# Kernel tuning notes

Hardware: AMD Instinct MI355X
Metric: run time of the kernel (lower is better)

Reference implementation:

```python
import jax, jax.numpy as jnp
import numpy as np

DIM = 512
HEADS = 8
DIM_HEAD = 64
HIDDEN = HEADS * DIM_HEAD  # 512


def setup_inputs() -> dict:
    key = jax.random.key(0)
    k1, k2, k3, k4 = jax.random.split(key, 4)
    x = jax.random.normal(k1, (8, DIM, 64, 64), dtype=jnp.float32)
    # 1x1 conv weights stored as [out_ch, in_ch] (kernel spatial dims are 1)
    w_qkv = jax.random.normal(k2, (HIDDEN * 3, DIM), dtype=jnp.float32) * (1.0 / np.sqrt(DIM))
    w_out = jax.random.normal(k3, (DIM, HIDDEN), dtype=jnp.float32) * (1.0 / np.sqrt(HIDDEN))
    b_out = jax.random.normal(k4, (DIM,), dtype=jnp.float32) * 0.01
    return {"x": x, "w_qkv": w_qkv, "w_out": w_out, "b_out": b_out}


def reference(x, w_qkv, w_out, b_out):
    b, c, h, w = x.shape
    n = h * w
    # to_qkv: 1x1 conv == per-pixel GEMM over channels
    qkv = jnp.einsum('bchw,oc->bohw', x, w_qkv)            # [b, 3*hidden, h, w]
    qkv = qkv.reshape(b, 3, HEADS, DIM_HEAD, n)            # matches torch reshape order
    q, k, v = qkv[:, 0], qkv[:, 1], qkv[:, 2]              # each [b, heads, dim_head, n]
    k = jax.nn.softmax(k, axis=-1)                          # softmax over spatial positions
    context = jnp.einsum('bhdn,bhen->bhde', k, v)          # [b, heads, d, e] kv outer-product
    out = jnp.einsum('bhde,bhdn->bhen', context, q)        # query readout [b, heads, e, n]
    out = out.reshape(b, HEADS * DIM_HEAD, h, w)
    # to_out: 1x1 conv with bias
    return jnp.einsum('bchw,oc->bohw', out, w_out) + b_out[None, :, None, None]
```

## Files before the change

### kernel.cpp

```cpp
#include <hip/hip_runtime.h>
#include <hip/hip_bf16.h>
#include <math.h>

#define NB    8
#define CDIM  512
#define NSP   4096
#define NHEAD 8

typedef short short8 __attribute__((ext_vector_type(8)));
typedef float f32x4  __attribute__((ext_vector_type(4)));

__device__ __forceinline__ unsigned short f2bf(float f) {
    unsigned int u = __float_as_uint(f);
    u += 0x7fff + ((u >> 16) & 1);
    return (unsigned short)(u >> 16);
}
__device__ __forceinline__ float bf2f(unsigned short s) {
    return __uint_as_float(((unsigned int)s) << 16);
}
__device__ __forceinline__ void gld_lds16(const void* g, void* s) {
    __builtin_amdgcn_global_load_lds(
        (const __attribute__((address_space(1))) unsigned int*)g,
        (__attribute__((address_space(3))) unsigned int*)s, 16, 0, 0);
}
__device__ __forceinline__ void split8(const float* s, short8& hi, short8& lo) {
    float4 a = *reinterpret_cast<const float4*>(s);
    float4 b = *reinterpret_cast<const float4*>(s + 4);
    float v[8] = {a.x, a.y, a.z, a.w, b.x, b.y, b.z, b.w};
    #pragma unroll
    for (int j = 0; j < 8; ++j) {
        unsigned short hh = f2bf(v[j]);
        hi[j] = (short)hh;
        lo[j] = (short)f2bf(v[j] - bf2f(hh));
    }
}

__global__ __launch_bounds__(256) void convert_x(const float* __restrict__ x,
    unsigned short* __restrict__ xh, unsigned short* __restrict__ xl)
{
    const int cb4 = blockIdx.x;
    const int kt  = blockIdx.y;
    const int b   = blockIdx.z;
    const int tid = threadIdx.x;

    __shared__ float sx[32][65];

    const int r  = tid >> 3;
    const int c8 = (tid & 7) * 8;
    const float* xp = x + ((long)b * CDIM + kt * 32 + r) * NSP + cb4 * 64 + c8;
    float4 v0 = *reinterpret_cast<const float4*>(xp);
    float4 v1 = *reinterpret_cast<const float4*>(xp + 4);
    sx[r][c8 + 0] = v0.x; sx[r][c8 + 1] = v0.y; sx[r][c8 + 2] = v0.z; sx[r][c8 + 3] = v0.w;
    sx[r][c8 + 4] = v1.x; sx[r][c8 + 5] = v1.y; sx[r][c8 + 6] = v1.z; sx[r][c8 + 7] = v1.w;
    __syncthreads();

    const int cb_l  = tid >> 6;
    const int lane  = tid & 63;
    const int cb    = cb4 * 4 + cb_l;
    const int col_l = cb_l * 16 + (lane & 15);
    const int k0    = (lane >> 4) * 8;
    short8 hv, lv;
    #pragma unroll
    for (int j = 0; j < 8; ++j) {
        float v = sx[k0 + j][col_l];
        unsigned short hh = f2bf(v);
        hv[j] = (short)hh;
        lv[j] = (short)f2bf(v - bf2f(hh));
    }
    const long base = (((long)(b * 256 + cb) * 16 + kt) * 512) + lane * 8;
    *reinterpret_cast<short8*>(xh + base) = hv;
    *reinterpret_cast<short8*>(xl + base) = lv;
}

__global__ __launch_bounds__(64) void convert_w(const float* __restrict__ w,
    unsigned short* __restrict__ wh, unsigned short* __restrict__ wl)
{
    const int lane = threadIdx.x & 63;
    const int rb = blockIdx.x;
    const int kt = blockIdx.y;
    const int row = rb * 16 + (lane & 15);
    const int k0  = kt * 32 + (lane >> 4) * 8;
    const float* wp = w + (long)row * CDIM + k0;
    const long base = ((long)rb * 16 + kt) * 512 + lane * 8;
    short8 hv, lv;
    #pragma unroll
    for (int j = 0; j < 8; ++j) {
        float v = wp[j];
        unsigned short h = f2bf(v);
        hv[j] = (short)h;
        lv[j] = (short)f2bf(v - bf2f(h));
    }
    *reinterpret_cast<short8*>(wh + base) = hv;
    *reinterpret_cast<short8*>(wl + base) = lv;
}

__global__ __launch_bounds__(64) void convert_b(const float* __restrict__ src,
    int ld, unsigned short* __restrict__ bh, unsigned short* __restrict__ bl)
{
    const int lane = threadIdx.x & 63;
    const int cb = blockIdx.x;
    const int kt = blockIdx.y;
    const int col = cb * 16 + (lane & 15);
    const int k0  = kt * 32 + (lane >> 4) * 8;
    const float* sp = src + (long)k0 * ld + col;
    const long base = ((long)cb * 16 + kt) * 512 + lane * 8;
    short8 hv, lv;
    #pragma unroll
    for (int j = 0; j < 8; ++j) {
        float v = sp[(long)j * ld];
        unsigned short h = f2bf(v);
        hv[j] = (short)h;
        lv[j] = (short)f2bf(v - bf2f(h));
    }
    *reinterpret_cast<short8*>(bh + base) = hv;
    *reinterpret_cast<short8*>(bl + base) = lv;
}

__global__ __launch_bounds__(256, 2) void fused_kv_ctx(
    const unsigned short* __restrict__ Ah, const unsigned short* __restrict__ Al,
    const unsigned short* __restrict__ Bh, const unsigned short* __restrict__ Bl,
    float* __restrict__ ctx, float* __restrict__ ssum)
{
    const int ch = blockIdx.x;
    const int h  = blockIdx.y;
    const int b  = blockIdx.z;
    const int tid  = threadIdx.x;
    const int lane = tid & 63;
    const int wid  = tid >> 6;
    const int wr = wid >> 1, wc = wid & 1;

    __shared__ __align__(16) char lds[49152];

    f32x4 acc[4][8];
    #pragma unroll
    for (int m = 0; m < 4; ++m)
        #pragma unroll
        for (int n = 0; n < 8; ++n)
            acc[m][n] = (f32x4){0.f, 0.f, 0.f, 0.f};

    const unsigned short* srcs[12];
    #pragma unroll
    for (int i = 0; i < 12; ++i) {
        const int blk = wid * 12 + i;
        const unsigned short* s;
        if (blk < 16) {
            const int sub = blk & 7;
            const int rb = (sub < 4) ? (h * 4 + sub) : (32 + h * 4 + (sub - 4));
            s = ((blk < 8) ? Ah : Al) + ((long)(rb * 16) << 9);
        } else {
            const int j = (blk - 16) & 15;
            const int cb = ch * 16 + j;
            s = ((blk < 32) ? Bh : Bl) + (((long)(b * 256 + cb) * 16) << 9);
        }
        srcs[i] = s + lane * 8;
    }

    for (int kt = 0; kt < 16; ++kt) {
        #pragma unroll
        for (int i = 0; i < 12; ++i) {
            gld_lds16(srcs[i], lds + (wid * 12 + i) * 1024);
            srcs[i] += 512;
        }
        __syncthreads();

        short8 ah[4], al[4];
        #pragma unroll
        for (int m = 0; m < 4; ++m) {
            ah[m] = *reinterpret_cast<const short8*>(lds +        (wr * 4 + m) * 1024 + lane * 16);
            al[m] = *reinterpret_cast<const short8*>(lds + 8192 + (wr * 4 + m) * 1024 + lane * 16);
        }
        #pragma unroll
        for (int n = 0; n < 8; ++n) {
            short8 bh = *reinterpret_cast<const short8*>(lds + 16384 + (wc * 8 + n) * 1024 + lane * 16);
            short8 bl = *reinterpret_cast<const short8*>(lds + 32768 + (wc * 8 + n) * 1024 + lane * 16);
            #pragma unroll
            for (int m = 0; m < 4; ++m) {
                acc[m][n] = __builtin_amdgcn_mfma_f32_16x16x32_bf16(ah[m], bh, acc[m][n], 0, 0, 0);
                acc[m][n] = __builtin_amdgcn_mfma_f32_16x16x32_bf16(ah[m], bl, acc[m][n], 0, 0, 0);
                acc[m][n] = __builtin_amdgcn_mfma_f32_16x16x32_bf16(al[m], bh, acc[m][n], 0, 0, 0);
            }
        }
        __syncthreads();
    }

    if (wr == 0) {
        #pragma unroll
        for (int m = 0; m < 4; ++m)
            #pragma unroll
            for (int j = 0; j < 4; ++j) {
                float s = 0.f;
                #pragma unroll
                for (int n = 0; n < 8; ++n) {
                    float e = __expf(acc[m][n][j]);
                    acc[m][n][j] = e;
                    s += e;
                }
                s += __shfl_xor(s, 1); s += __shfl_xor(s, 2);
                s += __shfl_xor(s, 4); s += __shfl_xor(s, 8);
                if ((lane & 15) == 0)
                    atomicAdd(&ssum[b * 512 + h * 64 + m * 16 + (lane >> 4) * 4 + j], s);
            }
    }

    float* Plds = (float*)lds;
    float* Vlds = (float*)(lds + 64 * 68 * 4);
    f32x4 acc2[2][2];
    #pragma unroll
    for (int mi = 0; mi < 2; ++mi)
        #pragma unroll
        for (int ni = 0; ni < 2; ++ni) acc2[mi][ni] = (f32x4){0.f, 0.f, 0.f, 0.f};

    #pragma unroll
    for (int q = 0; q < 4; ++q) {
        __syncthreads();
        if (wc == (q >> 1)) {
            float* T = (wr == 0) ? Plds : Vlds;
            #pragma unroll
            for (int m = 0; m < 4; ++m)
                #pragma unroll
                for (int nn = 0; nn < 4; ++nn)
                    #pragma unroll
                    for (int j = 0; j < 4; ++j)
                        T[(m * 16 + (lane >> 4) * 4 + j) * 68 + nn * 16 + (lane & 15)]
                            = acc[m][(q & 1) * 4 + nn][j];
        }
        __syncthreads();

        #pragma unroll
        for (int ks = 0; ks < 2; ++ks) {
            const int kcol = ks * 32 + (lane >> 4) * 8;
            short8 pa_h[2], pa_l[2], vb_h[2], vb_l[2];
            #pragma unroll
            for (int mi = 0; mi < 2; ++mi)
                split8(&Plds[((wr * 2 + mi) * 16 + (lane & 15)) * 68 + kcol], pa_h[mi], pa_l[mi]);
            #pragma unroll
            for (int ni = 0; ni < 2; ++ni)
                split8(&Vlds[((wc * 2 + ni) * 16 + (lane & 15)) * 68 + kcol], vb_h[ni], vb_l[ni]);
            #pragma unroll
            for (int mi = 0; mi < 2; ++mi)
                #pragma unroll
                for (int ni = 0; ni < 2; ++ni) {
                    acc2[mi][ni] = __builtin_amdgcn_mfma_f32_16x16x32_bf16(pa_h[mi], vb_h[ni], acc2[mi][ni], 0, 0, 0);
                    acc2[mi][ni] = __builtin_amdgcn_mfma_f32_16x16x32_bf16(pa_h[mi], vb_l[ni], acc2[mi][ni], 0, 0, 0);
                    acc2[mi][ni] = __builtin_amdgcn_mfma_f32_16x16x32_bf16(pa_l[mi], vb_h[ni], acc2[mi][ni], 0, 0, 0);
                }
        }
    }

    float* cp = ctx + (long)(b * NHEAD + h) * 4096;
    #pragma unroll
    for (int mi = 0; mi < 2; ++mi)
        #pragma unroll
        for (int ni = 0; ni < 2; ++ni) {
            const int d0 = (wr * 2 + mi) * 16;
            const int e0 = (wc * 2 + ni) * 16;
            #pragma unroll
            for (int j = 0; j < 4; ++j)
                atomicAdd(&cp[(d0 + (lane >> 4) * 4 + j) * 64 + e0 + (lane & 15)], acc2[mi][ni][j]);
        }
}

template<int NKT, bool BIAS>
__global__ __launch_bounds__(512, 2) void gemm_mfma256(
    const unsigned short* __restrict__ Ah, const unsigned short* __restrict__ Al,
    const unsigned short* __restrict__ Bh, const unsigned short* __restrict__ Bl,
    float* __restrict__ C, const float* __restrict__ bias,
    int N, int aBatchRB, int bBatchCB, long cBatch)
{
    const int b    = blockIdx.z;
    const int tid  = threadIdx.x;
    const int lane = tid & 63;
    const int wid  = tid >> 6;
    const int wr   = wid >> 2;
    const int wc   = wid & 3;

    __shared__ __align__(16) char lds[2][65536];

    f32x4 acc[8][4];
    #pragma unroll
    for (int m = 0; m < 8; ++m)
        #pragma unroll
        for (int n = 0; n < 4; ++n)
            acc[m][n] = (f32x4){0.f, 0.f, 0.f, 0.f};

    const int rb0 = b * aBatchRB + blockIdx.y * 16;
    const int cb0 = b * bBatchCB + blockIdx.x * 16;

    const unsigned short* srcs[8];
    #pragma unroll
    for (int i = 0; i < 8; ++i) {
        const int blk = wid * 8 + i;
        const int sub = blk & 15;
        const unsigned short* s;
        if (blk < 16)      s = Ah + ((long)(rb0 + sub) * NKT << 9);
        else if (blk < 32) s = Al + ((long)(rb0 + sub) * NKT << 9);
        else if (blk < 48) s = Bh + ((long)(cb0 + sub) * NKT << 9);
        else               s = Bl + ((long)(cb0 + sub) * NKT << 9);
        srcs[i] = s + lane * 8;
    }
    const int ldsoff = wid * 8192;

    #pragma unroll
    for (int i = 0; i < 8; ++i) {
        gld_lds16(srcs[i], &lds[0][ldsoff + i * 1024]);
        srcs[i] += 512;
    }

    int cur = 0;
    for (int kt = 0; kt < NKT; ++kt) {
        if (kt + 1 < NKT) {
            #pragma unroll
            for (int i = 0; i < 8; ++i) {
                gld_lds16(srcs[i], &lds[cur ^ 1][ldsoff + i * 1024]);
                srcs[i] += 512;
            }
            asm volatile("s_waitcnt vmcnt(8)" ::: "memory");
        } else {
            asm volatile("s_waitcnt vmcnt(0)" ::: "memory");
        }
        __builtin_amdgcn_s_barrier();

        const char* L = lds[cur];
        short8 ah[8], al[8];
        #pragma unroll
        for (int m = 0; m < 8; ++m) {
            ah[m] = *reinterpret_cast<const short8*>(L +         (wr * 8 + m) * 1024 + lane * 16);
            al[m] = *reinterpret_cast<const short8*>(L + 16384 + (wr * 8 + m) * 1024 + lane * 16);
        }
        __builtin_amdgcn_s_setprio(1);
        #pragma unroll
        for (int n = 0; n < 4; ++n) {
            short8 bh = *reinterpret_cast<const short8*>(L + 32768 + (wc * 4 + n) * 1024 + lane * 16);
            short8 bl = *reinterpret_cast<const short8*>(L + 49152 + (wc * 4 + n) * 1024 + lane * 16);
            #pragma unroll
            for (int m = 0; m < 8; ++m) {
                acc[m][n] = __builtin_amdgcn_mfma_f32_16x16x32_bf16(ah[m], bh, acc[m][n], 0, 0, 0);
                acc[m][n] = __builtin_amdgcn_mfma_f32_16x16x32_bf16(ah[m], bl, acc[m][n], 0, 0, 0);
                acc[m][n] = __builtin_amdgcn_mfma_f32_16x16x32_bf16(al[m], bh, acc[m][n], 0, 0, 0);
            }
        }
        __builtin_amdgcn_s_setprio(0);
        asm volatile("" ::: "memory");
        __builtin_amdgcn_s_barrier();
        asm volatile("" ::: "memory");
        cur ^= 1;
    }

    const int row0 = blockIdx.y * 256 + wr * 128;
    const int col0 = blockIdx.x * 256 + wc * 64;
    float* Cb = C + (long)b * cBatch;
    #pragma unroll
    for (int m = 0; m < 8; ++m)
        #pragma unroll
        for (int n = 0; n < 4; ++n) {
            const int col = col0 + n * 16 + (lane & 15);
            #pragma unroll
            for (int j = 0; j < 4; ++j) {
                const int row = row0 + m * 16 + (lane >> 4) * 4 + j;
                float v = acc[m][n][j];
                if (BIAS) v += bias[row];
                Cb[(long)row * N + col] = v;
            }
        }
}

template<int NKT, bool BIAS>
__global__ __launch_bounds__(256) void gemm_mfma(
    const unsigned short* __restrict__ Ah, const unsigned short* __restrict__ Al,
    const unsigned short* __restrict__ Bh, const unsigned short* __restrict__ Bl,
    float* __restrict__ C, const float* __restrict__ bias,
    int N, int aBatchRB, int bBatchCB, long cBatch)
{
    const int b    = blockIdx.z;
    const int tid  = threadIdx.x;
    const int lane = tid & 63;
    const int wid  = tid >> 6;
    const int wr   = wid >> 1;
    const int wc   = wid & 1;

    __shared__ __align__(16) char lds[32768];

    f32x4 acc[4][4];
    #pragma unroll
    for (int m = 0; m < 4; ++m)
        #pragma unroll
        for (int n = 0; n < 4; ++n)
            acc[m][n] = (f32x4){0.f, 0.f, 0.f, 0.f};

    const int rb0 = b * aBatchRB + blockIdx.y * 8;
    const int cb0 = b * bBatchCB + blockIdx.x * 8;

    const unsigned short* srcs[8];
    #pragma unroll
    for (int i = 0; i < 8; ++i) {
        const int blk = wid * 8 + i;
        const int sub = blk & 7;
        const unsigned short* s;
        if (blk < 8)       s = Ah + ((long)(rb0 + sub) * NKT << 9);
        else if (blk < 16) s = Al + ((long)(rb0 + sub) * NKT << 9);
        else if (blk < 24) s = Bh + ((long)(cb0 + sub) * NKT << 9);
        else               s = Bl + ((long)(cb0 + sub) * NKT << 9);
        srcs[i] = s + lane * 8;
    }

    for (int kt = 0; kt < NKT; ++kt) {
        #pragma unroll
        for (int i = 0; i < 8; ++i) {
            gld_lds16(srcs[i], lds + (wid * 8 + i) * 1024);
            srcs[i] += 512;
        }
        __syncthreads();

        short8 ah[4], al[4], bh[4], bl[4];
        #pragma unroll
        for (int m = 0; m < 4; ++m) {
            ah[m] = *reinterpret_cast<const short8*>(lds +         (wr * 4 + m) * 1024 + lane * 16);
            al[m] = *reinterpret_cast<const short8*>(lds +  8192 + (wr * 4 + m) * 1024 + lane * 16);
        }
        #pragma unroll
        for (int n = 0; n < 4; ++n) {
            bh[n] = *reinterpret_cast<const short8*>(lds + 16384 + (wc * 4 + n) * 1024 + lane * 16);
            bl[n] = *reinterpret_cast<const short8*>(lds + 24576 + (wc * 4 + n) * 1024 + lane * 16);
        }
        #pragma unroll
        for (int m = 0; m < 4; ++m)
            #pragma unroll
            for (int n = 0; n < 4; ++n) {
                acc[m][n] = __builtin_amdgcn_mfma_f32_16x16x32_bf16(ah[m], bh[n], acc[m][n], 0, 0, 0);
                acc[m][n] = __builtin_amdgcn_mfma_f32_16x16x32_bf16(ah[m], bl[n], acc[m][n], 0, 0, 0);
                acc[m][n] = __builtin_amdgcn_mfma_f32_16x16x32_bf16(al[m], bh[n], acc[m][n], 0, 0, 0);
            }
        __syncthreads();
    }

    const int row0 = blockIdx.y * 128 + wr * 64;
    const int col0 = blockIdx.x * 128 + wc * 64;
    float* Cb = C + (long)b * cBatch;
    #pragma unroll
    for (int m = 0; m < 4; ++m)
        #pragma unroll
        for (int n = 0; n < 4; ++n) {
            const int col = col0 + n * 16 + (lane & 15);
            #pragma unroll
            for (int j = 0; j < 4; ++j) {
                const int row = row0 + m * 16 + (lane >> 4) * 4 + j;
                float v = acc[m][n][j];
                if (BIAS) v += bias[row];
                Cb[(long)row * N + col] = v;
            }
        }
}

__global__ __launch_bounds__(256) void zero_buf(float* p, int n) {
    for (int i = blockIdx.x * 256 + threadIdx.x; i < n; i += gridDim.x * 256) p[i] = 0.f;
}

__global__ __launch_bounds__(256) void ctx_fold(
    const float* __restrict__ w_out, const float* __restrict__ ctx,
    const float* __restrict__ ssum, float* __restrict__ Amat)
{
    const int o0 = blockIdx.x * 64;
    const int h  = blockIdx.y;
    const int b  = blockIdx.z;
    const int tid = threadIdx.x;

    __shared__ float Wo[64][65];
    __shared__ float Ct[64][65];

    for (int idx = tid; idx < 64 * 16; idx += 256) {
        const int r = idx >> 4;
        const int c = (idx & 15) * 4;
        float4 w4 = *reinterpret_cast<const float4*>(&w_out[(long)(o0 + r) * CDIM + h * 64 + c]);
        Wo[r][c + 0] = w4.x; Wo[r][c + 1] = w4.y; Wo[r][c + 2] = w4.z; Wo[r][c + 3] = w4.w;
        float4 c4 = *reinterpret_cast<const float4*>(&ctx[(((long)(b * NHEAD + h) * 64 + r) * 64) + c]);
        Ct[r][c + 0] = c4.x; Ct[r][c + 1] = c4.y; Ct[r][c + 2] = c4.z; Ct[r][c + 3] = c4.w;
    }
    __syncthreads();

    const int to = tid >> 4, td = tid & 15;
    float acc[4][4];
    #pragma unroll
    for (int i = 0; i < 4; ++i)
        #pragma unroll
        for (int j = 0; j < 4; ++j) acc[i][j] = 0.f;

    for (int e = 0; e < 64; ++e) {
        float ro[4], rd[4];
        #pragma unroll
        for (int i = 0; i < 4; ++i) ro[i] = Wo[to * 4 + i][e];
        #pragma unroll
        for (int j = 0; j < 4; ++j) rd[j] = Ct[td * 4 + j][e];
        #pragma unroll
        for (int i = 0; i < 4; ++i)
            #pragma unroll
            for (int j = 0; j < 4; ++j) acc[i][j] += ro[i] * rd[j];
    }

    #pragma unroll
    for (int i = 0; i < 4; ++i)
        #pragma unroll
        for (int j = 0; j < 4; ++j) {
            const float s = 1.f / ssum[b * 512 + h * 64 + td * 4 + j];
            Amat[(long)b * CDIM * CDIM + (long)(o0 + to * 4 + i) * CDIM + h * 64 + td * 4 + j]
                = acc[i][j] * s;
        }
}

extern "C" void kernel_launch(void* const* d_in, const int* in_sizes, int n_in,
                              void* d_out, int out_size, void* d_ws, size_t ws_size,
                              hipStream_t stream) {
    (void)in_sizes; (void)n_in; (void)out_size; (void)ws_size;
    const float* x     = (const float*)d_in[0];
    const float* w_qkv = (const float*)d_in[1];
    const float* w_out = (const float*)d_in[2];
    const float* b_out = (const float*)d_in[3];
    float* out = (float*)d_out;

    char* ws = (char*)d_ws;
    unsigned short* xh   = (unsigned short*)(ws + 134217728L);
    unsigned short* xl   = (unsigned short*)(ws + 167772160L);
    unsigned short* wkvh = (unsigned short*)(ws + 201326592L);
    unsigned short* wkvl = (unsigned short*)(ws + 202375168L);
    float*          ssum = (float*)(ws + 203423744L);
    float*          ctx  = (float*)(ws + 203440128L);
    float*          Amat = (float*)(ws);
    float*          W3   = (float*)(ws + 8388608L);
    unsigned short* amh  = (unsigned short*)(ws + 16777216L);
    unsigned short* aml  = (unsigned short*)(ws + 20971520L);
    unsigned short* wqh  = (unsigned short*)(ws + 25165824L);
    unsigned short* wql  = (unsigned short*)(ws + 26214400L);
    unsigned short* w3h  = (unsigned short*)(ws + 27262976L);
    unsigned short* w3l  = (unsigned short*)(ws + 31457280L);

    convert_x<<<dim3(64, 16, NB), 256, 0, stream>>>(x, xh, xl);
    convert_w<<<dim3(64, 16), 64, 0, stream>>>(w_qkv + 512L * CDIM, wkvh, wkvl);
    zero_buf<<<256, 256, 0, stream>>>(ssum, (16384 + 1048576) / 4);

    fused_kv_ctx<<<dim3(16, NHEAD, NB), 256, 0, stream>>>(
        wkvh, wkvl, xh, xl, ctx, ssum);

    convert_b<<<dim3(32, 16), 64, 0, stream>>>(w_qkv, CDIM, wqh, wql);

    ctx_fold<<<dim3(8, NHEAD, NB), 256, 0, stream>>>(w_out, ctx, ssum, Amat);

    convert_w<<<dim3(256, 16), 64, 0, stream>>>(Amat, amh, aml);
    gemm_mfma<16, false><<<dim3(4, 4, NB), 256, 0, stream>>>(
        amh, aml, wqh, wql, W3, nullptr, CDIM, 32, 0, (long)CDIM * CDIM);

    convert_w<<<dim3(256, 16), 64, 0, stream>>>(W3, w3h, w3l);
    gemm_mfma256<16, true><<<dim3(16, 2, NB), 512, 0, stream>>>(
        w3h, w3l, xh, xl, out, b_out, NSP, 32, 256, (long)CDIM * NSP);
}
```

Before: 221.2 us.

## Rework kv-context kernel, split GEMM main loop into phases, fuse Amat bf16 split

```diff
diff --git a/kernel.cpp b/kernel.cpp
--- a/kernel.cpp
+++ b/kernel.cpp
@@ -116,152 +116,8 @@
     *reinterpret_cast<short8*>(bl + base) = lv;
 }
 
-__global__ __launch_bounds__(256, 2) void fused_kv_ctx(
-    const unsigned short* __restrict__ Ah, const unsigned short* __restrict__ Al,
-    const unsigned short* __restrict__ Bh, const unsigned short* __restrict__ Bl,
-    float* __restrict__ ctx, float* __restrict__ ssum)
-{
-    const int ch = blockIdx.x;
-    const int h  = blockIdx.y;
-    const int b  = blockIdx.z;
-    const int tid  = threadIdx.x;
-    const int lane = tid & 63;
-    const int wid  = tid >> 6;
-    const int wr = wid >> 1, wc = wid & 1;
-
-    __shared__ __align__(16) char lds[49152];
-
-    f32x4 acc[4][8];
-    #pragma unroll
-    for (int m = 0; m < 4; ++m)
-        #pragma unroll
-        for (int n = 0; n < 8; ++n)
-            acc[m][n] = (f32x4){0.f, 0.f, 0.f, 0.f};
-
-    const unsigned short* srcs[12];
-    #pragma unroll
-    for (int i = 0; i < 12; ++i) {
-        const int blk = wid * 12 + i;
-        const unsigned short* s;
-        if (blk < 16) {
-            const int sub = blk & 7;
-            const int rb = (sub < 4) ? (h * 4 + sub) : (32 + h * 4 + (sub - 4));
-            s = ((blk < 8) ? Ah : Al) + ((long)(rb * 16) << 9);
-        } else {
-            const int j = (blk - 16) & 15;
-            const int cb = ch * 16 + j;
-            s = ((blk < 32) ? Bh : Bl) + (((long)(b * 256 + cb) * 16) << 9);
-        }
-        srcs[i] = s + lane * 8;
-    }
-
-    for (int kt = 0; kt < 16; ++kt) {
-        #pragma unroll
-        for (int i = 0; i < 12; ++i) {
-            gld_lds16(srcs[i], lds + (wid * 12 + i) * 1024);
-            srcs[i] += 512;
-        }
-        __syncthreads();
-
-        short8 ah[4], al[4];
-        #pragma unroll
-        for (int m = 0; m < 4; ++m) {
-            ah[m] = *reinterpret_cast<const short8*>(lds +        (wr * 4 + m) * 1024 + lane * 16);
-            al[m] = *reinterpret_cast<const short8*>(lds + 8192 + (wr * 4 + m) * 1024 + lane * 16);
-        }
-        #pragma unroll
-        for (int n = 0; n < 8; ++n) {
-            short8 bh = *reinterpret_cast<const short8*>(lds + 16384 + (wc * 8 + n) * 1024 + lane * 16);
-            short8 bl = *reinterpret_cast<const short8*>(lds + 32768 + (wc * 8 + n) * 1024 + lane * 16);
-            #pragma unroll
-            for (int m = 0; m < 4; ++m) {
-                acc[m][n] = __builtin_amdgcn_mfma_f32_16x16x32_bf16(ah[m], bh, acc[m][n], 0, 0, 0);
-                acc[m][n] = __builtin_amdgcn_mfma_f32_16x16x32_bf16(ah[m], bl, acc[m][n], 0, 0, 0);
-                acc[m][n] = __builtin_amdgcn_mfma_f32_16x16x32_bf16(al[m], bh, acc[m][n], 0, 0, 0);
-            }
-        }
-        __syncthreads();
-    }
-
-    if (wr == 0) {
-        #pragma unroll
-        for (int m = 0; m < 4; ++m)
-            #pragma unroll
-            for (int j = 0; j < 4; ++j) {
-                float s = 0.f;
-                #pragma unroll
-                for (int n = 0; n < 8; ++n) {
-                    float e = __expf(acc[m][n][j]);
-                    acc[m][n][j] = e;
-                    s += e;
-                }
-                s += __shfl_xor(s, 1); s += __shfl_xor(s, 2);
-                s += __shfl_xor(s, 4); s += __shfl_xor(s, 8);
-                if ((lane & 15) == 0)
-                    atomicAdd(&ssum[b * 512 + h * 64 + m * 16 + (lane >> 4) * 4 + j], s);
-            }
-    }
-
-    float* Plds = (float*)lds;
-    float* Vlds = (float*)(lds + 64 * 68 * 4);
-    f32x4 acc2[2][2];
-    #pragma unroll
-    for (int mi = 0; mi < 2; ++mi)
-        #pragma unroll
-        for (int ni = 0; ni < 2; ++ni) acc2[mi][ni] = (f32x4){0.f, 0.f, 0.f, 0.f};
-
-    #pragma unroll
-    for (int q = 0; q < 4; ++q) {
-        __syncthreads();
-        if (wc == (q >> 1)) {
-            float* T = (wr == 0) ? Plds : Vlds;
-            #pragma unroll
-            for (int m = 0; m < 4; ++m)
-                #pragma unroll
-                for (int nn = 0; nn < 4; ++nn)
-                    #pragma unroll
-                    for (int j = 0; j < 4; ++j)
-                        T[(m * 16 + (lane >> 4) * 4 + j) * 68 + nn * 16 + (lane & 15)]
-                            = acc[m][(q & 1) * 4 + nn][j];
-        }
-        __syncthreads();
-
-        #pragma unroll
-        for (int ks = 0; ks < 2; ++ks) {
-            const int kcol = ks * 32 + (lane >> 4) * 8;
-            short8 pa_h[2], pa_l[2], vb_h[2], vb_l[2];
-            #pragma unroll
-            for (int mi = 0; mi < 2; ++mi)
-                split8(&Plds[((wr * 2 + mi) * 16 + (lane & 15)) * 68 + kcol], pa_h[mi], pa_l[mi]);
-            #pragma unroll
-            for (int ni = 0; ni < 2; ++ni)
-                split8(&Vlds[((wc * 2 + ni) * 16 + (lane & 15)) * 68 + kcol], vb_h[ni], vb_l[ni]);
-            #pragma unroll
-            for (int mi = 0; mi < 2; ++mi)
-                #pragma unroll
-                for (int ni = 0; ni < 2; ++ni) {
-                    acc2[mi][ni] = __builtin_amdgcn_mfma_f32_16x16x32_bf16(pa_h[mi], vb_h[ni], acc2[mi][ni], 0, 0, 0);
-                    acc2[mi][ni] = __builtin_amdgcn_mfma_f32_16x16x32_bf16(pa_h[mi], vb_l[ni], acc2[mi][ni], 0, 0, 0);
-                    acc2[mi][ni] = __builtin_amdgcn_mfma_f32_16x16x32_bf16(pa_l[mi], vb_h[ni], acc2[mi][ni], 0, 0, 0);
-                }
-        }
-    }
-
-    float* cp = ctx + (long)(b * NHEAD + h) * 4096;
-    #pragma unroll
-    for (int mi = 0; mi < 2; ++mi)
-        #pragma unroll
-        for (int ni = 0; ni < 2; ++ni) {
-            const int d0 = (wr * 2 + mi) * 16;
-            const int e0 = (wc * 2 + ni) * 16;
-            #pragma unroll
-            for (int j = 0; j < 4; ++j)
-                atomicAdd(&cp[(d0 + (lane >> 4) * 4 + j) * 64 + e0 + (lane & 15)], acc2[mi][ni][j]);
-        }
-}
-
 template<int NKT, bool BIAS>
-__global__ __launch_bounds__(512, 2) void gemm_mfma256(
+__global__ __launch_bounds__(512, 2) void gemm256_8ph(
     const unsigned short* __restrict__ Ah, const unsigned short* __restrict__ Al,
     const unsigned short* __restrict__ Bh, const unsigned short* __restrict__ Bl,
     float* __restrict__ C, const float* __restrict__ bias,
@@ -280,8 +136,7 @@
     #pragma unroll
     for (int m = 0; m < 8; ++m)
         #pragma unroll
-        for (int n = 0; n < 4; ++n)
-            acc[m][n] = (f32x4){0.f, 0.f, 0.f, 0.f};
+        for (int n = 0; n < 4; ++n) acc[m][n] = (f32x4){0.f, 0.f, 0.f, 0.f};
 
     const int rb0 = b * aBatchRB + blockIdx.y * 16;
     const int cb0 = b * bBatchCB + blockIdx.x * 16;
@@ -298,52 +153,58 @@
         else               s = Bl + ((long)(cb0 + sub) * NKT << 9);
         srcs[i] = s + lane * 8;
     }
-    const int ldsoff = wid * 8192;
 
     #pragma unroll
     for (int i = 0; i < 8; ++i) {
-        gld_lds16(srcs[i], &lds[0][ldsoff + i * 1024]);
+        gld_lds16(srcs[i], &lds[0][(wid * 8 + i) * 1024]);
         srcs[i] += 512;
     }
-
-    int cur = 0;
+    asm volatile("s_waitcnt vmcnt(0)" ::: "memory");
+    __builtin_amdgcn_s_barrier();
+    asm volatile("" ::: "memory");
+
     for (int kt = 0; kt < NKT; ++kt) {
-        if (kt + 1 < NKT) {
-            #pragma unroll
-            for (int i = 0; i < 8; ++i) {
-                gld_lds16(srcs[i], &lds[cur ^ 1][ldsoff + i * 1024]);
-                srcs[i] += 512;
-            }
-            asm volatile("s_waitcnt vmcnt(8)" ::: "memory");
-        } else {
-            asm volatile("s_waitcnt vmcnt(0)" ::: "memory");
-        }
-        __builtin_amdgcn_s_barrier();
-
-        const char* L = lds[cur];
-        short8 ah[8], al[8];
-        #pragma unroll
-        for (int m = 0; m < 8; ++m) {
-            ah[m] = *reinterpret_cast<const short8*>(L +         (wr * 8 + m) * 1024 + lane * 16);
-            al[m] = *reinterpret_cast<const short8*>(L + 16384 + (wr * 8 + m) * 1024 + lane * 16);
-        }
-        __builtin_amdgcn_s_setprio(1);
-        #pragma unroll
-        for (int n = 0; n < 4; ++n) {
-            short8 bh = *reinterpret_cast<const short8*>(L + 32768 + (wc * 4 + n) * 1024 + lane * 16);
-            short8 bl = *reinterpret_cast<const short8*>(L + 49152 + (wc * 4 + n) * 1024 + lane * 16);
-            #pragma unroll
-            for (int m = 0; m < 8; ++m) {
-                acc[m][n] = __builtin_amdgcn_mfma_f32_16x16x32_bf16(ah[m], bh, acc[m][n], 0, 0, 0);
-                acc[m][n] = __builtin_amdgcn_mfma_f32_16x16x32_bf16(ah[m], bl, acc[m][n], 0, 0, 0);
-                acc[m][n] = __builtin_amdgcn_mfma_f32_16x16x32_bf16(al[m], bh, acc[m][n], 0, 0, 0);
-            }
-        }
-        __builtin_amdgcn_s_setprio(0);
-        asm volatile("" ::: "memory");
-        __builtin_amdgcn_s_barrier();
-        asm volatile("" ::: "memory");
-        cur ^= 1;
+        const char* L = lds[kt & 1];
+        char* Ln = lds[(kt & 1) ^ 1];
+        short8 bh[4], bl[4];
+        #pragma unroll
+        for (int p = 0; p < 4; ++p) {
+            short8 ah0 = *reinterpret_cast<const short8*>(L +         (wr * 8 + 2 * p)     * 1024 + lane * 16);
+            short8 ah1 = *reinterpret_cast<const short8*>(L +         (wr * 8 + 2 * p + 1) * 1024 + lane * 16);
+            short8 al0 = *reinterpret_cast<const short8*>(L + 16384 + (wr * 8 + 2 * p)     * 1024 + lane * 16);
+            short8 al1 = *reinterpret_cast<const short8*>(L + 16384 + (wr * 8 + 2 * p + 1) * 1024 + lane * 16);
+            if (p == 0) {
+                #pragma unroll
+                for (int n = 0; n < 4; ++n) {
+                    bh[n] = *reinterpret_cast<const short8*>(L + 32768 + (wc * 4 + n) * 1024 + lane * 16);
+                    bl[n] = *reinterpret_cast<const short8*>(L + 49152 + (wc * 4 + n) * 1024 + lane * 16);
+                }
+                if (kt + 1 < NKT) {
+                    #pragma unroll
+                    for (int i = 0; i < 8; ++i) {
+                        gld_lds16(srcs[i], &Ln[(wid * 8 + i) * 1024]);
+                        srcs[i] += 512;
+                    }
+                }
+            }
+            __builtin_amdgcn_s_barrier();
+            asm volatile("s_waitcnt lgkmcnt(0)" ::: "memory");
+            __builtin_amdgcn_s_setprio(1);
+            #pragma unroll
+            for (int n = 0; n < 4; ++n) {
+                acc[2*p  ][n] = __builtin_amdgcn_mfma_f32_16x16x32_bf16(ah0, bh[n], acc[2*p  ][n], 0, 0, 0);
+                acc[2*p  ][n] = __builtin_amdgcn_mfma_f32_16x16x32_bf16(ah0, bl[n], acc[2*p  ][n], 0, 0, 0);
+                acc[2*p  ][n] = __builtin_amdgcn_mfma_f32_16x16x32_bf16(al0, bh[n], acc[2*p  ][n], 0, 0, 0);
+                acc[2*p+1][n] = __builtin_amdgcn_mfma_f32_16x16x32_bf16(ah1, bh[n], acc[2*p+1][n], 0, 0, 0);
+                acc[2*p+1][n] = __builtin_amdgcn_mfma_f32_16x16x32_bf16(ah1, bl[n], acc[2*p+1][n], 0, 0, 0);
+                acc[2*p+1][n] = __builtin_amdgcn_mfma_f32_16x16x32_bf16(al1, bh[n], acc[2*p+1][n], 0, 0, 0);
+            }
+            __builtin_amdgcn_s_setprio(0);
+            if (p == 3 && kt + 1 < NKT)
+                asm volatile("s_waitcnt vmcnt(0)" ::: "memory");
+            __builtin_amdgcn_s_barrier();
+            asm volatile("" ::: "memory");
+        }
     }
 
     const int row0 = blockIdx.y * 256 + wr * 128;
@@ -362,6 +223,173 @@
                 Cb[(long)row * N + col] = v;
             }
         }
+}
+
+__global__ __launch_bounds__(512, 2) void fused_kv_ctx2(
+    const unsigned short* __restrict__ Ah, const unsigned short* __restrict__ Al,
+    const unsigned short* __restrict__ Bh, const unsigned short* __restrict__ Bl,
+    float* __restrict__ ctx, float* __restrict__ ssum)
+{
+    const int ch = blockIdx.x;
+    const int h0 = blockIdx.y * 2;
+    const int b  = blockIdx.z;
+    const int tid  = threadIdx.x;
+    const int lane = tid & 63;
+    const int wid  = tid >> 6;
+    const int wr   = wid >> 2;
+    const int wc   = wid & 3;
+
+    __shared__ __align__(16) char lds[2][65536];
+
+    f32x4 acc[8][4];
+    #pragma unroll
+    for (int m = 0; m < 8; ++m)
+        #pragma unroll
+        for (int n = 0; n < 4; ++n) acc[m][n] = (f32x4){0.f, 0.f, 0.f, 0.f};
+
+    const unsigned short* srcs[8];
+    #pragma unroll
+    for (int i = 0; i < 8; ++i) {
+        const int blk = wid * 8 + i;
+        const int sub = blk & 15;
+        int rb;
+        if (sub < 8) rb = (h0 + (sub >> 2)) * 4 + (sub & 3);
+        else         rb = 32 + (h0 + ((sub - 8) >> 2)) * 4 + ((sub - 8) & 3);
+        const unsigned short* s;
+        if (blk < 16)      s = Ah + ((long)rb * 16 << 9);
+        else if (blk < 32) s = Al + ((long)rb * 16 << 9);
+        else {
+            const int cb = ch * 16 + (blk & 15);
+            s = ((blk < 48) ? Bh : Bl) + (((long)(b * 256 + cb) * 16) << 9);
+        }
+        srcs[i] = s + lane * 8;
+    }
+
+    #pragma unroll
+    for (int i = 0; i < 8; ++i) {
+        gld_lds16(srcs[i], &lds[0][(wid * 8 + i) * 1024]);
+        srcs[i] += 512;
+    }
+    asm volatile("s_waitcnt vmcnt(0)" ::: "memory");
+    __builtin_amdgcn_s_barrier();
+    asm volatile("" ::: "memory");
+
+    for (int kt = 0; kt < 16; ++kt) {
+        const char* L = lds[kt & 1];
+        char* Ln = lds[(kt & 1) ^ 1];
+        short8 bh[4], bl[4];
+        #pragma unroll
+        for (int p = 0; p < 4; ++p) {
+            short8 ah0 = *reinterpret_cast<const short8*>(L +         (wr * 8 + 2 * p)     * 1024 + lane * 16);
+            short8 ah1 = *reinterpret_cast<const short8*>(L +         (wr * 8 + 2 * p + 1) * 1024 + lane * 16);
+            short8 al0 = *reinterpret_cast<const short8*>(L + 16384 + (wr * 8 + 2 * p)     * 1024 + lane * 16);
+            short8 al1 = *reinterpret_cast<const short8*>(L + 16384 + (wr * 8 + 2 * p + 1) * 1024 + lane * 16);
+            if (p == 0) {
+                #pragma unroll
+                for (int n = 0; n < 4; ++n) {
+                    bh[n] = *reinterpret_cast<const short8*>(L + 32768 + (wc * 4 + n) * 1024 + lane * 16);
+                    bl[n] = *reinterpret_cast<const short8*>(L + 49152 + (wc * 4 + n) * 1024 + lane * 16);
+                }
+                if (kt + 1 < 16) {
+                    #pragma unroll
+                    for (int i = 0; i < 8; ++i) {
+                        gld_lds16(srcs[i], &Ln[(wid * 8 + i) * 1024]);
+                        srcs[i] += 512;
+                    }
+                }
+            }
+            __builtin_amdgcn_s_barrier();
+            asm volatile("s_waitcnt lgkmcnt(0)" ::: "memory");
+            __builtin_amdgcn_s_setprio(1);
+            #pragma unroll
+            for (int n = 0; n < 4; ++n) {
+                acc[2*p  ][n] = __builtin_amdgcn_mfma_f32_16x16x32_bf16(ah0, bh[n], acc[2*p  ][n], 0, 0, 0);
+                acc[2*p  ][n] = __builtin_amdgcn_mfma_f32_16x16x32_bf16(ah0, bl[n], acc[2*p  ][n], 0, 0, 0);
+                acc[2*p  ][n] = __builtin_amdgcn_mfma_f32_16x16x32_bf16(al0, bh[n], acc[2*p  ][n], 0, 0, 0);
+                acc[2*p+1][n] = __builtin_amdgcn_mfma_f32_16x16x32_bf16(ah1, bh[n], acc[2*p+1][n], 0, 0, 0);
+                acc[2*p+1][n] = __builtin_amdgcn_mfma_f32_16x16x32_bf16(ah1, bl[n], acc[2*p+1][n], 0, 0, 0);
+                acc[2*p+1][n] = __builtin_amdgcn_mfma_f32_16x16x32_bf16(al1, bh[n], acc[2*p+1][n], 0, 0, 0);
+            }
+            __builtin_amdgcn_s_setprio(0);
+            if (p == 3 && kt + 1 < 16)
+                asm volatile("s_waitcnt vmcnt(0)" ::: "memory");
+            __builtin_amdgcn_s_barrier();
+            asm volatile("" ::: "memory");
+        }
+    }
+
+    if (wr == 0) {
+        #pragma unroll
+        for (int m = 0; m < 8; ++m)
+            #pragma unroll
+            for (int j = 0; j < 4; ++j) {
+                float s = 0.f;
+                #pragma unroll
+                for (int n = 0; n < 4; ++n) {
+                    float e = __expf(acc[m][n][j]);
+                    acc[m][n][j] = e;
+                    s += e;
+                }
+                s += __shfl_xor(s, 1); s += __shfl_xor(s, 2);
+                s += __shfl_xor(s, 4); s += __shfl_xor(s, 8);
+                if ((lane & 15) == 0)
+                    atomicAdd(&ssum[b * 512 + (h0 + (m >> 2)) * 64 + (m & 3) * 16 + (lane >> 4) * 4 + j], s);
+            }
+    }
+
+    float* Plds = (float*)&lds[0][0];
+    float* Vlds = (float*)(&lds[0][0] + 64 * 68 * 4);
+    #pragma unroll
+    for (int hh = 0; hh < 2; ++hh) {
+        f32x4 acc2[2][2];
+        #pragma unroll
+        for (int mi = 0; mi < 2; ++mi)
+            #pragma unroll
+            for (int ni = 0; ni < 2; ++ni) acc2[mi][ni] = (f32x4){0.f, 0.f, 0.f, 0.f};
+
+        #pragma unroll
+        for (int q = 0; q < 4; ++q) {
+            __syncthreads();
+            if (wc == q) {
+                float* T = (wr == 0) ? Plds : Vlds;
+                #pragma unroll
+                for (int m = 0; m < 4; ++m)
+                    #pragma unroll
+                    for (int n = 0; n < 4; ++n)
+                        #pragma unroll
+                        for (int j = 0; j < 4; ++j)
+                            T[(m * 16 + (lane >> 4) * 4 + j) * 68 + n * 16 + (lane & 15)]
+                                = acc[hh * 4 + m][n][j];
+            }
+            __syncthreads();
+            const int kcol = (wc >> 1) * 32 + (lane >> 4) * 8;
+            short8 pa_h[2], pa_l[2], vb_h[2], vb_l[2];
+            #pragma unroll
+            for (int mi = 0; mi < 2; ++mi)
+                split8(&Plds[((wr * 2 + mi) * 16 + (lane & 15)) * 68 + kcol], pa_h[mi], pa_l[mi]);
+            #pragma unroll
+            for (int ni = 0; ni < 2; ++ni)
+                split8(&Vlds[(((wc & 1) * 2 + ni) * 16 + (lane & 15)) * 68 + kcol], vb_h[ni], vb_l[ni]);
+            #pragma unroll
+            for (int mi = 0; mi < 2; ++mi)
+                #pragma unroll
+                for (int ni = 0; ni < 2; ++ni) {
+                    acc2[mi][ni] = __builtin_amdgcn_mfma_f32_16x16x32_bf16(pa_h[mi], vb_h[ni], acc2[mi][ni], 0, 0, 0);
+                    acc2[mi][ni] = __builtin_amdgcn_mfma_f32_16x16x32_bf16(pa_h[mi], vb_l[ni], acc2[mi][ni], 0, 0, 0);
+                    acc2[mi][ni] = __builtin_amdgcn_mfma_f32_16x16x32_bf16(pa_l[mi], vb_h[ni], acc2[mi][ni], 0, 0, 0);
+                }
+        }
+        float* cp = ctx + (long)(b * NHEAD + h0 + hh) * 4096;
+        #pragma unroll
+        for (int mi = 0; mi < 2; ++mi)
+            #pragma unroll
+            for (int ni = 0; ni < 2; ++ni) {
+                #pragma unroll
+                for (int j = 0; j < 4; ++j)
+                    atomicAdd(&cp[((wr * 2 + mi) * 16 + (lane >> 4) * 4 + j) * 64
+                                  + ((wc & 1) * 2 + ni) * 16 + (lane & 15)], acc2[mi][ni][j]);
+            }
+    }
 }
 
 template<int NKT, bool BIAS>
@@ -384,8 +412,7 @@
     #pragma unroll
     for (int m = 0; m < 4; ++m)
         #pragma unroll
-        for (int n = 0; n < 4; ++n)
-            acc[m][n] = (f32x4){0.f, 0.f, 0.f, 0.f};
+        for (int n = 0; n < 4; ++n) acc[m][n] = (f32x4){0.f, 0.f, 0.f, 0.f};
 
     const int rb0 = b * aBatchRB + blockIdx.y * 8;
     const int cb0 = b * bBatchCB + blockIdx.x * 8;
@@ -455,9 +482,10 @@
     for (int i = blockIdx.x * 256 + threadIdx.x; i < n; i += gridDim.x * 256) p[i] = 0.f;
 }
 
-__global__ __launch_bounds__(256) void ctx_fold(
+__global__ __launch_bounds__(256) void ctx_fold2(
     const float* __restrict__ w_out, const float* __restrict__ ctx,
-    const float* __restrict__ ssum, float* __restrict__ Amat)
+    const float* __restrict__ ssum,
+    unsigned short* __restrict__ amh, unsigned short* __restrict__ aml)
 {
     const int o0 = blockIdx.x * 64;
     const int h  = blockIdx.y;
@@ -466,6 +494,7 @@
 
     __shared__ float Wo[64][65];
     __shared__ float Ct[64][65];
+    __shared__ float At[64][65];
 
     for (int idx = tid; idx < 64 * 16; idx += 256) {
         const int r = idx >> 4;
@@ -497,13 +526,29 @@
     }
 
     #pragma unroll
-    for (int i = 0; i < 4; ++i)
-        #pragma unroll
-        for (int j = 0; j < 4; ++j) {
-            const float s = 1.f / ssum[b * 512 + h * 64 + td * 4 + j];
-            Amat[(long)b * CDIM * CDIM + (long)(o0 + to * 4 + i) * CDIM + h * 64 + td * 4 + j]
-                = acc[i][j] * s;
-        }
+    for (int j = 0; j < 4; ++j) {
+        const float s = 1.f / ssum[b * 512 + h * 64 + td * 4 + j];
+        #pragma unroll
+        for (int i = 0; i < 4; ++i)
+            At[to * 4 + i][td * 4 + j] = acc[i][j] * s;
+    }
+    __syncthreads();
+
+    const int g = tid >> 6, lane = tid & 63;
+    #pragma unroll
+    for (int kt_l = 0; kt_l < 2; ++kt_l) {
+        short8 hv, lv;
+        #pragma unroll
+        for (int jj = 0; jj < 8; ++jj) {
+            float v = At[g * 16 + (lane & 15)][kt_l * 32 + (lane >> 4) * 8 + jj];
+            unsigned short hh = f2bf(v);
+            hv[jj] = (short)hh;
+            lv[jj] = (short)f2bf(v - bf2f(hh));
+        }
+        const long base = (((long)(b * 32 + (o0 >> 4) + g) * 16) + (h * 2 + kt_l)) * 512 + lane * 8;
+        *reinterpret_cast<short8*>(amh + base) = hv;
+        *reinterpret_cast<short8*>(aml + base) = lv;
+    }
 }
 
 extern "C" void kernel_launch(void* const* d_in, const int* in_sizes, int n_in,
@@ -523,7 +568,6 @@
     unsigned short* wkvl = (unsigned short*)(ws + 202375168L);
     float*          ssum = (float*)(ws + 203423744L);
     float*          ctx  = (float*)(ws + 203440128L);
-    float*          Amat = (float*)(ws);
     float*          W3   = (float*)(ws + 8388608L);
     unsigned short* amh  = (unsigned short*)(ws + 16777216L);
     unsigned short* aml  = (unsigned short*)(ws + 20971520L);
@@ -536,18 +580,17 @@
     convert_w<<<dim3(64, 16), 64, 0, stream>>>(w_qkv + 512L * CDIM, wkvh, wkvl);
     zero_buf<<<256, 256, 0, stream>>>(ssum, (16384 + 1048576) / 4);
 
-    fused_kv_ctx<<<dim3(16, NHEAD, NB), 256, 0, stream>>>(
+    fused_kv_ctx2<<<dim3(16, 4, NB), 512, 0, stream>>>(
         wkvh, wkvl, xh, xl, ctx, ssum);
 
     convert_b<<<dim3(32, 16), 64, 0, stream>>>(w_qkv, CDIM, wqh, wql);
 
-    ctx_fold<<<dim3(8, NHEAD, NB), 256, 0, stream>>>(w_out, ctx, ssum, Amat);
-
-    convert_w<<<dim3(256, 16), 64, 0, stream>>>(Amat, amh, aml);
+    ctx_fold2<<<dim3(8, NHEAD, NB), 256, 0, stream>>>(w_out, ctx, ssum, amh, aml);
+
     gemm_mfma<16, false><<<dim3(4, 4, NB), 256, 0, stream>>>(
         amh, aml, wqh, wql, W3, nullptr, CDIM, 32, 0, (long)CDIM * CDIM);
 
     convert_w<<<dim3(256, 16), 64, 0, stream>>>(W3, w3h, w3l);
-    gemm_mfma256<16, true><<<dim3(16, 2, NB), 512, 0, stream>>>(
+    gemm256_8ph<16, true><<<dim3(16, 2, NB), 512, 0, stream>>>(
         w3h, w3l, xh, xl, out, b_out, NSP, 32, 256, (long)CDIM * NSP);
 }
```

Result: slower. 240.1 us (+8.6%).
